# Optimization experiments

Measured on AMD Instinct MI355X. Metric: run time of the kernel, lower is better.

## Reference

```python
import jax, jax.numpy as jnp
import numpy as np

B, T, E = 4, 2048, 1024
H = 16
D = E // H  # head_dim = 64


def setup_inputs() -> dict:
    key = jax.random.key(0)
    k1, k2, k3 = jax.random.split(key, 3)
    x = jax.random.normal(k1, (B, T, E), dtype=jnp.float32)
    # torch nn.Linear weights: y = x @ W.T ; init scaled like uniform fan_in
    W_qkv = jax.random.normal(k2, (3 * E, E), dtype=jnp.float32) * (E ** -0.5)
    W_out = jax.random.normal(k3, (E, E), dtype=jnp.float32) * (E ** -0.5)
    return {"x": x, "W_qkv": W_qkv, "W_out": W_out}


def reference(x, W_qkv, W_out):
    b, t, c = x.shape
    scale = D ** -0.5
    qkv = jnp.einsum('btc,fc->btf', x, W_qkv)          # [B,T,3E]
    q, k, v = jnp.split(qkv, 3, axis=-1)
    # [B,H,T,D]
    q = q.reshape(b, t, H, D).transpose(0, 2, 1, 3)
    k = k.reshape(b, t, H, D).transpose(0, 2, 1, 3)
    v = v.reshape(b, t, H, D).transpose(0, 2, 1, 3)
    attn = jnp.einsum('bhqd,bhkd->bhqk', q, k) * scale  # [B,H,T,T]
    causal = jnp.triu(jnp.ones((t, t), dtype=bool), k=1)
    attn = jnp.where(causal, -jnp.inf, attn)
    attn = jax.nn.softmax(attn, axis=-1)
    out = jnp.einsum('bhqk,bhkd->bhqd', attn, v)        # [B,H,T,D]
    out = out.transpose(0, 2, 1, 3).reshape(b, t, c)
    return jnp.einsum('btc,oc->bto', out, W_out)
```

## Files before the change

kernel.cpp:

```cpp
#include <hip/hip_runtime.h>

using u16 = unsigned short;
using u32 = unsigned int;
typedef __bf16 bf16;
typedef bf16 bf16x8 __attribute__((ext_vector_type(8)));
typedef u16 u16x8 __attribute__((ext_vector_type(8)));
typedef u16 u16x4 __attribute__((ext_vector_type(4)));
typedef u32 u32x2 __attribute__((ext_vector_type(2)));
typedef float f32x4 __attribute__((ext_vector_type(4)));

#define LDSS 72

__device__ __forceinline__ u16 f2bf(float f) {
  u32 u = __builtin_bit_cast(u32, f);
  u += 0x7FFFu + ((u >> 16) & 1u);
  return (u16)(u >> 16);
}

__device__ __forceinline__ u32 packtrunc(float lo, float hi) {
  return __builtin_amdgcn_perm(__builtin_bit_cast(u32, hi),
                               __builtin_bit_cast(u32, lo), 0x07060302u);
}

__device__ __forceinline__ float fexp2(float x) {
#if __has_builtin(__builtin_amdgcn_exp2f)
  return __builtin_amdgcn_exp2f(x);
#else
  return exp2f(x);
#endif
}

__device__ __forceinline__ bf16x8 ldfrag(const u16* p) {
  return __builtin_bit_cast(bf16x8, *(const u16x8*)p);
}

__device__ __forceinline__ u16x8 cvt8(const float* p) {
  float4 a = ((const float4*)p)[0];
  float4 b = ((const float4*)p)[1];
  u16x8 o;
  o[0] = f2bf(a.x); o[1] = f2bf(a.y); o[2] = f2bf(a.z); o[3] = f2bf(a.w);
  o[4] = f2bf(b.x); o[5] = f2bf(b.y); o[6] = f2bf(b.z); o[7] = f2bf(b.w);
  return o;
}

__device__ __forceinline__ void gll16(const u16* g, u16* l) {
  __builtin_amdgcn_global_load_lds(
      (const __attribute__((address_space(1))) u32*)g,
      (__attribute__((address_space(3))) u32*)l, 16, 0, 0);
}

__global__ __launch_bounds__(256) void cvt_bf16(
    const float* __restrict__ src, u16* __restrict__ dst, int n8) {
  int i = blockIdx.x * 256 + threadIdx.x;
  const int stride = gridDim.x * 256;
  for (; i < n8; i += stride)
    ((u16x8*)dst)[i] = cvt8(&src[(size_t)i * 8]);
}

template<int MODE, int NBX>
__global__ __launch_bounds__(512) void gemm128(
    const u16* __restrict__ Ag, const u16* __restrict__ Bg,
    u16* __restrict__ Qw, u16* __restrict__ Kw, u16* __restrict__ Vtw,
    float* __restrict__ Og) {
  extern __shared__ u16 lds[];
  u16* Ab0 = lds;
  u16* Bb0 = lds + 8192;
  u16* Ab1 = lds + 24576;
  u16* Bb1 = lds + 32768;

  const int tid = threadIdx.x;
  const int lane = tid & 63;
  const int wid = tid >> 6;
  const int wm = wid >> 2, wn = wid & 3;
  const int quad = lane >> 4, l16 = lane & 15;
  const int lr = lane >> 3;
  const int csrc = ((lane & 7) * 8) ^ (lr << 3);
  const int swl = (l16 & 7) << 3;

  const int nwg = NBX * 64;
  const int cpx = nwg >> 3;
  const int bid = blockIdx.x;
  const int swz = (bid & 7) * cpx + (bid >> 3);
  const int by = swz / NBX, bx = swz % NBX;
  const int arow0 = by * 128, brow0 = bx * 256;

  f32x4 acc[4][4] = {};

  auto stg = [&](int t, u16* Abuf, u16* Bbuf) {
#pragma unroll
    for (int s2 = 0; s2 < 2; ++s2) {
      int r = s2 * 64 + wid * 8;
      gll16(&Ag[(size_t)(arow0 + r + lr) * 1024 + t * 64 + csrc], &Abuf[r * 64]);
    }
#pragma unroll
    for (int s2 = 0; s2 < 4; ++s2) {
      int r = s2 * 64 + wid * 8;
      gll16(&Bg[(size_t)(brow0 + r + lr) * 1024 + t * 64 + csrc], &Bbuf[r * 64]);
    }
  };

  stg(0, Ab0, Bb0);

#define RD_B(J2) do { \
  _Pragma("unroll") for (int kk = 0; kk < 2; ++kk) \
    bfx[((J2) & 1) * 2 + kk + (((J2) >> 1) << 2)] = ldfrag( \
        &Bc[(wn * 64 + (J2) * 16 + l16) * 64 + ((kk * 32 + quad * 8) ^ swl)]); \
} while(0)
#define RD_A(I2, MH) do { \
  _Pragma("unroll") for (int kk = 0; kk < 2; ++kk) \
    af[(I2) * 2 + kk] = ldfrag( \
        &Ac[(wm * 64 + ((MH) * 2 + (I2)) * 16 + l16) * 64 + ((kk * 32 + quad * 8) ^ swl)]); \
} while(0)
#define FENCE do { asm volatile("s_waitcnt lgkmcnt(0)" ::: "memory"); \
                   __builtin_amdgcn_sched_barrier(0); } while(0)
#define MM(MH, J2, BI) do { \
  __builtin_amdgcn_s_setprio(1); \
  _Pragma("unroll") for (int i2 = 0; i2 < 2; ++i2) \
  _Pragma("unroll") for (int j2 = 0; j2 < 2; ++j2) \
  _Pragma("unroll") for (int kk = 0; kk < 2; ++kk) \
    acc[(MH) * 2 + i2][(J2) + j2] = __builtin_amdgcn_mfma_f32_16x16x32_bf16( \
        af[i2 * 2 + kk], bfx[(BI) + j2 * 2 + kk], acc[(MH) * 2 + i2][(J2) + j2], 0, 0, 0); \
  __builtin_amdgcn_s_setprio(0); \
  __builtin_amdgcn_sched_barrier(0); \
} while(0)

  auto body = [&](const u16* Ac, const u16* Bc, u16* An, u16* Bn, int t) {
    asm volatile("s_waitcnt lgkmcnt(0)" ::: "memory");
    __builtin_amdgcn_s_barrier();
    if (t + 1 < 16) {
      stg(t + 1, An, Bn);
      asm volatile("s_waitcnt vmcnt(6)" ::: "memory");
    } else {
      asm volatile("s_waitcnt vmcnt(0)" ::: "memory");
    }
    __builtin_amdgcn_s_barrier();

    bf16x8 bfx[8], af[4];
    RD_B(0); RD_B(1); RD_A(0, 0); RD_A(1, 0);
    FENCE; MM(0, 0, 0);
    RD_B(2); RD_B(3);
    FENCE; MM(0, 2, 4);
    RD_A(0, 1); RD_A(1, 1);
    FENCE; MM(1, 2, 4);
    MM(1, 0, 0);
  };

  for (int t = 0; t < 16; t += 2) {
    body(Ab0, Bb0, Ab1, Bb1, t);
    body(Ab1, Bb1, Ab0, Bb0, t + 1);
  }
#undef RD_B
#undef RD_A
#undef FENCE
#undef MM

  if constexpr (MODE == 0) {
    const int part = bx >> 2;
    const int h = (bx & 3) * 4 + wn;
    const int bb = by >> 4;
    const int t0 = (by & 15) * 128 + wm * 64;
    if (part < 2) {
      u16* dst = part == 0 ? Qw : Kw;
      const float qs = part == 0 ? 0.18033688011112042f : 1.0f;
      const size_t rowb = (size_t)(bb * 16 + h) * 2048;
#pragma unroll
      for (int i2 = 0; i2 < 4; ++i2)
#pragma unroll
        for (int j2 = 0; j2 < 4; ++j2) {
          int tt = t0 + i2 * 16 + quad * 4;
          int d = j2 * 16 + l16;
#pragma unroll
          for (int r = 0; r < 4; ++r)
            dst[(rowb + tt + r) * 64 + d] = f2bf(acc[i2][j2][r] * qs);
        }
    } else {
      __builtin_amdgcn_s_barrier();
      u16* tb = lds + wid * 4096;
#pragma unroll
      for (int i2 = 0; i2 < 4; ++i2)
#pragma unroll
        for (int j2 = 0; j2 < 4; ++j2) {
          u16x4 v4;
#pragma unroll
          for (int r = 0; r < 4; ++r) v4[r] = f2bf(acc[i2][j2][r]);
          int mb = i2 * 16 + quad * 4;
          *(u16x4*)&tb[(j2 * 16 + l16) * 64 + (mb ^ (l16 << 2))] = v4;
        }
      asm volatile("s_waitcnt lgkmcnt(0)" ::: "memory");
      const int dl = lane;
      const int swr = (dl & 15) << 2;
      u16* vr = Vtw + ((size_t)(bb * 16 + h) * 64 + dl) * 2048 + t0;
#pragma unroll
      for (int c8 = 0; c8 < 8; ++c8) {
        u16x4 q0 = *(u16x4*)&tb[dl * 64 + ((c8 * 8) ^ swr)];
        u16x4 q1 = *(u16x4*)&tb[dl * 64 + ((c8 * 8 + 4) ^ swr)];
        u16x8 o;
        o[0] = q0[0]; o[1] = q0[1]; o[2] = q0[2]; o[3] = q0[3];
        o[4] = q1[0]; o[5] = q1[1]; o[6] = q1[2]; o[7] = q1[3];
        *(u16x8*)&vr[c8 * 8] = o;
      }
    }
  } else {
    const size_t mrow = (size_t)arow0 + wm * 64;
    const int ocol = brow0 + wn * 64;
#pragma unroll
    for (int i2 = 0; i2 < 4; ++i2)
#pragma unroll
      for (int j2 = 0; j2 < 4; ++j2)
#pragma unroll
        for (int r = 0; r < 4; ++r)
          Og[(mrow + i2 * 16 + quad * 4 + r) * 1024 + ocol + j2 * 16 + l16] =
              acc[i2][j2][r];
  }
}

__global__ __launch_bounds__(256) void attn_kernel(
    const u16* __restrict__ Qw, const u16* __restrict__ Kw,
    const u16* __restrict__ Vtw, u16* __restrict__ Ao) {
  __shared__ u16 kbuf0[64 * 64], vbuf0[64 * 64];
  __shared__ u16 kbuf1[64 * 64], vbuf1[64 * 64];
  __shared__ u16 pws[4][32 * LDSS];
  const int tid = threadIdx.x;
  const int lane = tid & 63;
  const int wid = tid >> 6;
  const int quad = lane >> 4;
  const int l16 = lane & 15;
  const int g = 15 - (int)(blockIdx.x >> 6);
  const int bh = blockIdx.x & 63;
  const u16* Qb = Qw + (size_t)bh * 2048 * 64;
  const u16* Kb = Kw + (size_t)bh * 2048 * 64;
  const u16* Vb = Vtw + (size_t)bh * 64 * 2048;
  const int sq = 4 * g + wid;
  const int qrow0 = sq * 32;
  const int nktw = (sq >> 1) + 1;
  const int nkt = 2 * g + 2;
  u16* pw = pws[wid];

  const int lr = lane >> 3;
  const int lsw = ((lane & 7) * 8) ^ (lr << 3);
  const int sx = (l16 & 7) << 3;

  bf16x8 qf[2][2];
#pragma unroll
  for (int i = 0; i < 2; ++i)
#pragma unroll
    for (int kk = 0; kk < 2; ++kk)
      qf[i][kk] = ldfrag(&Qb[(size_t)(qrow0 + i * 16 + l16) * 64 + kk * 32 + quad * 8]);

  f32x4 oacc[4][2] = {};
  float lacc[2] = {0.f, 0.f};
  const f32x4 minit = {-8.f, -8.f, -8.f, -8.f};

  auto stage = [&](int kt, u16* kb, u16* vb) {
    const u16* Kt = Kb + (size_t)kt * 4096;
    const u16* Vt = Vb + kt * 64;
#pragma unroll
    for (int c = 0; c < 2; ++c) {
      int base = wid * 1024 + c * 512;
      int rb = wid * 16 + c * 8;
      gll16(&Kt[(size_t)rb * 64 + lr * 64 + lsw], &kb[base]);
      gll16(&Vt[(size_t)rb * 2048 + lr * 2048 + lsw], &vb[base]);
    }
  };

  stage(0, kbuf0, vbuf0);

  auto body = [&](const u16* kc, const u16* vc, u16* kn, u16* vn, int kt) {
    asm volatile("s_waitcnt lgkmcnt(0)" ::: "memory");
    __builtin_amdgcn_s_barrier();
    const bool more = (kt + 1 < nkt);
    if (more) {
      stage(kt + 1, kn, vn);
      asm volatile("s_waitcnt vmcnt(4)" ::: "memory");
    } else {
      asm volatile("s_waitcnt vmcnt(0)" ::: "memory");
    }
    __builtin_amdgcn_s_barrier();
    if (kt >= nktw) return;

    f32x4 sv[2][4];
#pragma unroll
    for (int i = 0; i < 2; ++i)
#pragma unroll
      for (int j = 0; j < 4; ++j) sv[i][j] = minit;
    __builtin_amdgcn_s_setprio(1);
#pragma unroll
    for (int kk = 0; kk < 2; ++kk) {
      const int cq = (kk * 32 + quad * 8) ^ sx;
      bf16x8 kf[4];
#pragma unroll
      for (int j = 0; j < 4; ++j)
        kf[j] = ldfrag(&kc[(j * 16 + l16) * 64 + cq]);
#pragma unroll
      for (int i = 0; i < 2; ++i)
#pragma unroll
        for (int j = 0; j < 4; ++j)
          sv[i][j] = __builtin_amdgcn_mfma_f32_16x16x32_bf16(kf[j], qf[i][kk], sv[i][j], 0, 0, 0);
    }
    __builtin_amdgcn_s_setprio(0);

    if (kt * 64 + 63 > qrow0) {
#pragma unroll
      for (int i = 0; i < 2; ++i) {
        int q = qrow0 + i * 16 + l16;
#pragma unroll
        for (int j = 0; j < 4; ++j)
#pragma unroll
          for (int r = 0; r < 4; ++r)
            if (kt * 64 + j * 16 + quad * 4 + r > q) sv[i][j][r] = -INFINITY;
      }
    }

#pragma unroll
    for (int i = 0; i < 2; ++i) {
      float rs = 0.f;
#pragma unroll
      for (int j = 0; j < 4; ++j) {
        float p0 = fexp2(sv[i][j][0]);
        float p1 = fexp2(sv[i][j][1]);
        float p2 = fexp2(sv[i][j][2]);
        float p3 = fexp2(sv[i][j][3]);
        rs += (p0 + p1) + (p2 + p3);
        u32x2 pk;
        pk[0] = packtrunc(p0, p1);
        pk[1] = packtrunc(p2, p3);
        *(u32x2*)&pw[(i * 16 + l16) * LDSS + j * 16 + quad * 4] = pk;
      }
      lacc[i] += rs;
    }

#pragma unroll
    for (int kk = 0; kk < 2; ++kk) {
      const int cq = (kk * 32 + quad * 8) ^ sx;
      bf16x8 pf[2];
#pragma unroll
      for (int i = 0; i < 2; ++i)
        pf[i] = ldfrag(&pw[(i * 16 + l16) * LDSS + kk * 32 + quad * 8]);
      __builtin_amdgcn_s_setprio(1);
#pragma unroll
      for (int d = 0; d < 4; ++d) {
        bf16x8 vfd = ldfrag(&vc[(d * 16 + l16) * 64 + cq]);
#pragma unroll
        for (int i = 0; i < 2; ++i)
          oacc[d][i] = __builtin_amdgcn_mfma_f32_16x16x32_bf16(vfd, pf[i], oacc[d][i], 0, 0, 0);
      }
      __builtin_amdgcn_s_setprio(0);
    }
  };

  for (int kt = 0; kt < nkt; kt += 2) {
    body(kbuf0, vbuf0, kbuf1, vbuf1, kt);
    body(kbuf1, vbuf1, kbuf0, vbuf0, kt + 1);
  }

  const int bb = bh >> 4, h = bh & 15;
#pragma unroll
  for (int i = 0; i < 2; ++i) {
    float l = lacc[i];
    l += __shfl_xor(l, 16);
    l += __shfl_xor(l, 32);
    float inv = 1.f / l;
#pragma unroll
    for (int d = 0; d < 4; ++d) {
      u16x4 ok;
#pragma unroll
      for (int r = 0; r < 4; ++r) ok[r] = f2bf(oacc[d][i][r] * inv);
      *(u16x4*)&pw[(i * 16 + l16) * LDSS + d * 16 + quad * 4] = ok;
    }
  }
  __builtin_amdgcn_s_waitcnt(0);
  const int row = lane >> 1, half = lane & 1;
  const int t = qrow0 + row;
#pragma unroll
  for (int c = 0; c < 4; ++c) {
    u16x8 v = *(u16x8*)&pw[row * LDSS + half * 32 + c * 8];
    *(u16x8*)&Ao[((size_t)(bb * 2048 + t)) * 1024 + h * 64 + half * 32 + c * 8] = v;
  }
}

extern "C" void kernel_launch(void* const* d_in, const int* in_sizes, int n_in,
                              void* d_out, int out_size, void* d_ws, size_t ws_size,
                              hipStream_t stream) {
  (void)in_sizes; (void)n_in; (void)out_size; (void)ws_size;
  const float* x    = (const float*)d_in[0];
  const float* Wqkv = (const float*)d_in[1];
  const float* Wout = (const float*)d_in[2];
  float* out = (float*)d_out;
  u16* ws = (u16*)d_ws;

  const size_t NX   = (size_t)4 * 2048 * 1024;
  const size_t NQKV = (size_t)3072 * 1024;
  const size_t NOUT = (size_t)1024 * 1024;
  const size_t SZ   = NX;

  u16* Xc    = ws;
  u16* Wqkvc = Xc + NX;
  u16* Woutc = Wqkvc + NQKV;
  u16* Qw    = Woutc + NOUT;
  u16* Kw    = Qw + SZ;
  u16* Vtw   = Kw + SZ;
  u16* Ao    = Vtw + SZ;

  static bool attr_done = false;
  if (!attr_done) {
    (void)hipFuncSetAttribute(reinterpret_cast<const void*>(&gemm128<0, 12>),
                              hipFuncAttributeMaxDynamicSharedMemorySize, 98304);
    (void)hipFuncSetAttribute(reinterpret_cast<const void*>(&gemm128<1, 4>),
                              hipFuncAttributeMaxDynamicSharedMemorySize, 98304);
    attr_done = true;
  }

  cvt_bf16<<<dim3(1024), 256, 0, stream>>>(x, Xc, (int)(NX / 8));
  cvt_bf16<<<dim3(384), 256, 0, stream>>>(Wqkv, Wqkvc, (int)(NQKV / 8));
  cvt_bf16<<<dim3(128), 256, 0, stream>>>(Wout, Woutc, (int)(NOUT / 8));

  gemm128<0, 12><<<dim3(768), 512, 98304, stream>>>(
      Xc, Wqkvc, Qw, Kw, Vtw, nullptr);
  attn_kernel<<<dim3(1024), 256, 0, stream>>>(Qw, Kw, Vtw, Ao);
  gemm128<1, 4><<<dim3(256), 512, 98304, stream>>>(
      Ao, Woutc, nullptr, nullptr, nullptr, out);
}
```

Baseline: 232.7 us.

## Fuse input conversions into one launch and compute softmax row sums via MFMA

```diff
diff --git a/kernel.cpp b/kernel.cpp
--- a/kernel.cpp
+++ b/kernel.cpp
@@ -49,12 +49,20 @@
       (__attribute__((address_space(3))) u32*)l, 16, 0, 0);
 }
 
-__global__ __launch_bounds__(256) void cvt_bf16(
-    const float* __restrict__ src, u16* __restrict__ dst, int n8) {
+__global__ __launch_bounds__(256) void cvt_all(
+    const float* __restrict__ x, const float* __restrict__ wqkv,
+    const float* __restrict__ wout, u16* __restrict__ dst,
+    int nx8, int nq8, int no8) {
   int i = blockIdx.x * 256 + threadIdx.x;
   const int stride = gridDim.x * 256;
-  for (; i < n8; i += stride)
-    ((u16x8*)dst)[i] = cvt8(&src[(size_t)i * 8]);
+  const int total = nx8 + nq8 + no8;
+  for (; i < total; i += stride) {
+    const float* src; int j;
+    if (i < nx8)            { src = x;    j = i; }
+    else if (i < nx8 + nq8) { src = wqkv; j = i - nx8; }
+    else                    { src = wout; j = i - nx8 - nq8; }
+    ((u16x8*)dst)[i] = cvt8(&src[(size_t)j * 8]);
+  }
 }
 
 template<int MODE, int NBX>
@@ -247,8 +255,13 @@
     for (int kk = 0; kk < 2; ++kk)
       qf[i][kk] = ldfrag(&Qb[(size_t)(qrow0 + i * 16 + l16) * 64 + kk * 32 + quad * 8]);
 
+  u16x8 ones16;
+#pragma unroll
+  for (int e = 0; e < 8; ++e) ones16[e] = 0x3F80;
+  const bf16x8 onesf = __builtin_bit_cast(bf16x8, ones16);
+
   f32x4 oacc[4][2] = {};
-  float lacc[2] = {0.f, 0.f};
+  f32x4 lfr[2] = {};
   const f32x4 minit = {-8.f, -8.f, -8.f, -8.f};
 
   auto stage = [&](int kt, u16* kb, u16* vb) {
@@ -313,20 +326,17 @@
 
 #pragma unroll
     for (int i = 0; i < 2; ++i) {
-      float rs = 0.f;
 #pragma unroll
       for (int j = 0; j < 4; ++j) {
         float p0 = fexp2(sv[i][j][0]);
         float p1 = fexp2(sv[i][j][1]);
         float p2 = fexp2(sv[i][j][2]);
         float p3 = fexp2(sv[i][j][3]);
-        rs += (p0 + p1) + (p2 + p3);
         u32x2 pk;
         pk[0] = packtrunc(p0, p1);
         pk[1] = packtrunc(p2, p3);
         *(u32x2*)&pw[(i * 16 + l16) * LDSS + j * 16 + quad * 4] = pk;
       }
-      lacc[i] += rs;
     }
 
 #pragma unroll
@@ -337,6 +347,9 @@
       for (int i = 0; i < 2; ++i)
         pf[i] = ldfrag(&pw[(i * 16 + l16) * LDSS + kk * 32 + quad * 8]);
       __builtin_amdgcn_s_setprio(1);
+#pragma unroll
+      for (int i = 0; i < 2; ++i)
+        lfr[i] = __builtin_amdgcn_mfma_f32_16x16x32_bf16(onesf, pf[i], lfr[i], 0, 0, 0);
 #pragma unroll
       for (int d = 0; d < 4; ++d) {
         bf16x8 vfd = ldfrag(&vc[(d * 16 + l16) * 64 + cq]);
@@ -356,10 +369,7 @@
   const int bb = bh >> 4, h = bh & 15;
 #pragma unroll
   for (int i = 0; i < 2; ++i) {
-    float l = lacc[i];
-    l += __shfl_xor(l, 16);
-    l += __shfl_xor(l, 32);
-    float inv = 1.f / l;
+    float inv = 1.f / lfr[i][0];
 #pragma unroll
     for (int d = 0; d < 4; ++d) {
       u16x4 ok;
@@ -410,9 +420,8 @@
     attr_done = true;
   }
 
-  cvt_bf16<<<dim3(1024), 256, 0, stream>>>(x, Xc, (int)(NX / 8));
-  cvt_bf16<<<dim3(384), 256, 0, stream>>>(Wqkv, Wqkvc, (int)(NQKV / 8));
-  cvt_bf16<<<dim3(128), 256, 0, stream>>>(Wout, Woutc, (int)(NOUT / 8));
+  cvt_all<<<dim3(2048), 256, 0, stream>>>(
+      x, Wqkv, Wout, ws, (int)(NX / 8), (int)(NQKV / 8), (int)(NOUT / 8));
 
   gemm128<0, 12><<<dim3(768), 512, 98304, stream>>>(
       Xc, Wqkvc, Qw, Kw, Vtw, nullptr);
```

Measured after the change: 227.0 us. 2.5% less time.
